# Optimization experiments

Hardware: AMD Instinct MI355X
Metric: run time of the kernel (lower is better)

The kernel has to match this reference:

```python
import jax, jax.numpy as jnp
import numpy as np

NUM_HEADS = 8
MASK_NEG = -1e30


def setup_inputs() -> dict:
    key = jax.random.key(0)
    k1, k2, k3 = jax.random.split(key, 3)
    B, S, D = 8, 2048, 128
    queries = jax.random.normal(k1, (B, S, D), dtype=jnp.float32)
    mask = jnp.ones((B, S), dtype=jnp.float32)
    # kernel_size=1 Conv1D with no bias == dense matmul over last dim
    W_q = jax.random.normal(k2, (D, D), dtype=jnp.float32) * (D ** -0.5)
    W_mem = jax.random.normal(k3, (D, 2 * D), dtype=jnp.float32) * (D ** -0.5)
    return {"queries": queries, "mask": mask, "W_q": W_q, "W_mem": W_mem}


def _split_heads(x, h):
    # [B, S, D] -> [B, h, S, D/h]
    B, S, D = x.shape
    return x.reshape(B, S, h, D // h).transpose(0, 2, 1, 3)


def reference(queries, mask, W_q, W_mem):
    B, S, D = queries.shape
    h = NUM_HEADS
    scale = (D // h) ** -0.5
    memory = jnp.einsum('bsd,de->bse', queries, W_mem)   # [B,S,2D]
    query = jnp.einsum('bsd,de->bse', queries, W_q)      # [B,S,D]
    K, V = jnp.split(memory, 2, axis=2)
    Q = _split_heads(query, h) * scale                   # [B,h,S,dh]
    K = _split_heads(K, h)
    V = _split_heads(V, h)
    logits = jnp.einsum('bhqd,bhkd->bhqk', Q, K)         # [B,h,S,S]
    m = mask.reshape(B, 1, 1, S)
    logits = logits + (1.0 - m) * MASK_NEG
    weights = jax.nn.softmax(logits, axis=-1)
    # dropout is identity at inference (training=None)
    x = jnp.einsum('bhqk,bhkd->bhqd', weights, V)        # [B,h,S,dh]
    return x.transpose(0, 2, 1, 3).reshape(B, S, D)
```

## Files before the change

kernel.cpp:

```cpp
#include <hip/hip_runtime.h>
#include <hip/hip_bf16.h>
#include <stdint.h>

#define B_    8
#define S_    2048
#define D_    128
#define H_    8
#define DH_   16
#define BH_   64
#define E_    384
#define NT_   (S_ / 32)

typedef __attribute__((ext_vector_type(4)))  short short4v;
typedef __attribute__((ext_vector_type(8)))  short short8;
typedef __attribute__((ext_vector_type(4)))  float f32x4;
typedef __attribute__((ext_vector_type(16))) float f32x16;

__device__ inline unsigned short f2b(float f) {
    union { __bf16 h; unsigned short u; } t;
    t.h = (__bf16)f;
    return t.u;
}
__device__ inline float b2f(unsigned short u) {
    union { unsigned u; float f; } x; x.u = ((unsigned)u) << 16; return x.f;
}
__device__ inline int dperm(int d) {
    return (d & 3) | ((d & 8) >> 1) | ((d & 4) << 1);
}

__device__ inline void gload_lds16(const void* g, void* l) {
    __builtin_amdgcn_global_load_lds(
        (const __attribute__((address_space(1))) unsigned int*)g,
        (__attribute__((address_space(3))) unsigned int*)l, 16, 0, 0);
}

#define EXPB 16250.7346f

__global__ void wtrans_kernel(const float* __restrict__ Wq,
                              const float* __restrict__ Wmem,
                              unsigned short* __restrict__ wt) {
    int e = blockIdx.x, k = threadIdx.x;
    float v = (e < 128) ? Wq[k * 128 + e] : Wmem[k * 256 + (e - 128)];
    wt[e * 128 + k] = f2b(v);
}

__global__ __launch_bounds__(512) void proj_kernel(
        const float* __restrict__ X, const float* __restrict__ mask,
        const unsigned short* __restrict__ wt,
        unsigned short* __restrict__ Qb, unsigned short* __restrict__ KVf) {
    __shared__ unsigned short Xs[64][136];
    __shared__ unsigned short Vs[64][136];
    __shared__ float Ms[64];
    const int tid = threadIdx.x;
    const int b = blockIdx.x & 7, st = blockIdx.x >> 3;
    const int s0 = st * 64;
    const float* Xp = X + ((size_t)b * S_ + s0) * D_;

    for (int i = tid; i < 64 * D_ / 4; i += 512) {
        f32x4 v = __builtin_nontemporal_load((const f32x4*)Xp + i);
        int row = i >> 5, c4 = (i & 31) * 4;
        Xs[row][c4 + 0] = f2b(v[0]); Xs[row][c4 + 1] = f2b(v[1]);
        Xs[row][c4 + 2] = f2b(v[2]); Xs[row][c4 + 3] = f2b(v[3]);
    }
    if (tid < 64) Ms[tid] = mask[(size_t)b * S_ + s0 + tid];
    __syncthreads();

    const int wid = tid >> 6, lane = tid & 63;
    const int lr = lane & 15, lg = lane >> 4;
    const float qscale = 0.25f * 1.44269504088896f;

    for (int ci = 0; ci < 3; ++ci) {
        const int ct = wid + ci * 8;
        const int e0 = ct * 16;
        short4v bfr[8];
        #pragma unroll
        for (int kk = 0; kk < 8; ++kk)
            bfr[kk] = *(const short4v*)&wt[(e0 + lr) * 128 + kk * 16 + lg * 4];
        for (int rt = 0; rt < 4; ++rt) {
            f32x4 acc; acc[0] = acc[1] = acc[2] = acc[3] = 0.f;
            #pragma unroll
            for (int kk = 0; kk < 8; ++kk) {
                short4v a = *(const short4v*)&Xs[rt * 16 + lr][kk * 16 + lg * 4];
                acc = __builtin_amdgcn_mfma_f32_16x16x16bf16_1k(a, bfr[kk], acc, 0, 0, 0);
            }
            const int e = e0 + lr;
            #pragma unroll
            for (int r = 0; r < 4; ++r) {
                const int sl = rt * 16 + lg * 4 + r;
                const float v = acc[r];
                if (e < 128) {
                    int hh = e >> 4, d = dperm(e & 15);
                    Qb[(((size_t)b * H_ + hh) * S_ + s0 + sl) * DH_ + d] = f2b(v * qscale);
                } else if (e < 256) {
                    int ek = e - 128, hh = ek >> 4, d = dperm(ek & 15);
                    int T = st * 2 + (sl >> 5), qq = sl & 31;
                    int l = qq + 32 * (d >> 3), j = d & 7;
                    KVf[((size_t)(b * H_ + hh) * NT_ + T) * 1536 + l * 8 + j] = f2b(v);
                } else {
                    Vs[sl][e - 256] = f2b(v);
                }
            }
        }
    }
    __syncthreads();

    for (int j = tid; j < H_ * 2 * 2 * 64; j += 512) {
        const int l = j & 63, f = (j >> 6) & 1, t = (j >> 7) & 1, hh = j >> 8;
        const int q = l & 31, h = l >> 5;
        const int vrow = (q < 16) ? q : 16;
        const int T = st * 2 + t;
        unsigned short* dst =
            KVf + ((size_t)(b * H_ + hh) * NT_ + T) * 1536 + (1 + f) * 512 + l * 8;
        union { unsigned short us[8]; short8 v; } o;
        #pragma unroll
        for (int e = 0; e < 8; ++e) {
            const int p = f * 16 + 8 * h + e;
            const int sl = (p & 16) | dperm(p & 15);
            const int srow = t * 32 + sl;
            const float mk = Ms[srow];
            o.us[e] = f2b((vrow == 16) ? mk : b2f(Vs[srow][hh * 16 + vrow]) * mk);
        }
        *(short8*)dst = o.v;
    }
}

__global__ __launch_bounds__(512, 6) void attn_kernel(
        const unsigned short* __restrict__ Qb, const unsigned short* __restrict__ KVf,
        float* __restrict__ out) {
    const int tid = threadIdx.x;
    const int wid = tid >> 6, lane = tid & 63;
    const int q = lane & 31, h = lane >> 5;
    const int p = blockIdx.x;
    const int bh = (p & 7) * 8 + ((p >> 3) & 7);
    const int qt = p >> 6;
    const int q0 = qt * 128 + (wid >> 1) * 32;
    const int ttBase = (wid & 1) * (NT_ / 2);
    const int ttEnd  = ttBase + NT_ / 2;

    __shared__ unsigned short lds[8][2][3][64][8];

    const unsigned short* kv = KVf + (size_t)bh * NT_ * 1536 + (size_t)lane * 8;

    const short8 qf = *(const short8*)&Qb[((size_t)bh * S_ + q0 + q) * DH_ + 8 * h];

    f32x16 acc, z;
    #pragma unroll
    for (int i = 0; i < 16; ++i) { acc[i] = 0.f; z[i] = 0.f; }

#define STAGE(TT_, SL_)                                                        \
    {                                                                          \
        const unsigned short* g_ = kv + (size_t)(TT_) * 1536;                  \
        gload_lds16(g_,        &lds[wid][SL_][0][0][0]);                       \
        gload_lds16(g_ + 512,  &lds[wid][SL_][1][0][0]);                       \
        gload_lds16(g_ + 1024, &lds[wid][SL_][2][0][0]);                       \
    }

    STAGE(ttBase, 0); STAGE(ttBase + 1, 1);

    #pragma unroll 2
    for (int j = 0; j < 32; ++j) {
        const int slot = j & 1;
        asm volatile("s_waitcnt vmcnt(3)" ::: "memory");
        __builtin_amdgcn_sched_barrier(0);
        const short8 kf  = *(const short8*)&lds[wid][slot][0][lane][0];
        const short8 va0 = *(const short8*)&lds[wid][slot][1][lane][0];
        const short8 va1 = *(const short8*)&lds[wid][slot][2][lane][0];
        asm volatile("s_waitcnt lgkmcnt(0)" ::: "memory");
        __builtin_amdgcn_sched_barrier(0);
        const int nt2 = ttBase + j + 2;
        STAGE(nt2 < ttEnd ? nt2 : nt2 - 32, slot);

        __builtin_amdgcn_s_setprio(1);
        f32x16 s0 = __builtin_amdgcn_mfma_f32_32x32x16_bf16(kf, qf, z, 0, 0, 0);
        __builtin_amdgcn_s_setprio(0);

        union { unsigned u[4]; short8 v; } b0, b1;
        #pragma unroll
        for (int i = 0; i < 4; ++i) {
            const int l0 = (int)__builtin_fmaf(s0[2 * i],     128.f, EXPB);
            const int h0 = (int)__builtin_fmaf(s0[2 * i + 1], 128.f, EXPB);
            b0.u[i] = (unsigned)l0 | ((unsigned)h0 << 16);
            const int l1 = (int)__builtin_fmaf(s0[8 + 2 * i],     128.f, EXPB);
            const int h1 = (int)__builtin_fmaf(s0[8 + 2 * i + 1], 128.f, EXPB);
            b1.u[i] = (unsigned)l1 | ((unsigned)h1 << 16);
        }
        __builtin_amdgcn_s_setprio(1);
        acc = __builtin_amdgcn_mfma_f32_32x32x16_bf16(va0, b0.v, acc, 0, 0, 0);
        acc = __builtin_amdgcn_mfma_f32_32x32x16_bf16(va1, b1.v, acc, 0, 0, 0);
        __builtin_amdgcn_s_setprio(0);
    }
#undef STAGE

    asm volatile("s_waitcnt vmcnt(0)" ::: "memory");
    __syncthreads();

    float (*cmb)[16][64] = (float (*)[16][64]) & lds[0][0][0][0][0];
    if (wid & 1) {
        #pragma unroll
        for (int i = 0; i < 16; ++i)
            cmb[wid >> 1][i][lane] = acc[i];
    }
    __syncthreads();
    if (!(wid & 1)) {
        const int b = bh >> 3, head = bh & 7;
        float* obase = out + ((size_t)b * S_ + q0 + q) * D_ + head * DH_ + 4 * h;
        float o[16];
        #pragma unroll
        for (int i = 0; i < 16; ++i) o[i] = acc[i] + cmb[wid >> 1][i][lane];
        const float r = 1.0f / o[8];
        *(float4*)obase       = make_float4(o[0] * r, o[1] * r, o[2] * r, o[3] * r);
        *(float4*)(obase + 8) = make_float4(o[4] * r, o[5] * r, o[6] * r, o[7] * r);
    }
}

extern "C" void kernel_launch(void* const* d_in, const int* in_sizes, int n_in,
                              void* d_out, int out_size, void* d_ws, size_t ws_size,
                              hipStream_t stream) {
    const float* X    = (const float*)d_in[0];
    const float* mask = (const float*)d_in[1];
    const float* Wq   = (const float*)d_in[2];
    const float* Wmem = (const float*)d_in[3];
    float* out = (float*)d_out;

    unsigned short* Qb  = (unsigned short*)d_ws;
    unsigned short* KVf = Qb + (size_t)BH_ * S_ * DH_;
    unsigned short* wt  = KVf + (size_t)BH_ * NT_ * 1536;

    wtrans_kernel<<<E_, 128, 0, stream>>>(Wq, Wmem, wt);
    proj_kernel<<<B_ * S_ / 64, 512, 0, stream>>>(X, mask, wt, Qb, KVf);
    attn_kernel<<<BH_ * (S_ / 128), 512, 0, stream>>>(Qb, KVf, out);
}
```

Measured before the change: 63.84 us.

## Share KV tiles across all waves in block via cooperative LDS staging

```diff
diff --git a/kernel.cpp b/kernel.cpp
--- a/kernel.cpp
+++ b/kernel.cpp
@@ -124,7 +124,7 @@
     }
 }
 
-__global__ __launch_bounds__(512, 6) void attn_kernel(
+__global__ __launch_bounds__(512, 4) void attn_kernel(
         const unsigned short* __restrict__ Qb, const unsigned short* __restrict__ KVf,
         float* __restrict__ out) {
     const int tid = threadIdx.x;
@@ -132,85 +132,83 @@
     const int q = lane & 31, h = lane >> 5;
     const int p = blockIdx.x;
     const int bh = (p & 7) * 8 + ((p >> 3) & 7);
-    const int qt = p >> 6;
-    const int q0 = qt * 128 + (wid >> 1) * 32;
-    const int ttBase = (wid & 1) * (NT_ / 2);
-    const int ttEnd  = ttBase + NT_ / 2;
-
-    __shared__ unsigned short lds[8][2][3][64][8];
+    const int qs = p >> 6;
+    const int q0 = qs * 256 + wid * 32;
+
+    __shared__ unsigned short buf[2][8][3][64][8];
 
     const unsigned short* kv = KVf + (size_t)bh * NT_ * 1536 + (size_t)lane * 8;
 
     const short8 qf = *(const short8*)&Qb[((size_t)bh * S_ + q0 + q) * DH_ + 8 * h];
 
-    f32x16 acc, z;
+    f32x16 accA, accB, z;
     #pragma unroll
-    for (int i = 0; i < 16; ++i) { acc[i] = 0.f; z[i] = 0.f; }
-
-#define STAGE(TT_, SL_)                                                        \
+    for (int i = 0; i < 16; ++i) { accA[i] = 0.f; accB[i] = 0.f; z[i] = 0.f; }
+
+#define STAGE(C_)                                                              \
     {                                                                          \
-        const unsigned short* g_ = kv + (size_t)(TT_) * 1536;                  \
-        gload_lds16(g_,        &lds[wid][SL_][0][0][0]);                       \
-        gload_lds16(g_ + 512,  &lds[wid][SL_][1][0][0]);                       \
-        gload_lds16(g_ + 1024, &lds[wid][SL_][2][0][0]);                       \
-    }
-
-    STAGE(ttBase, 0); STAGE(ttBase + 1, 1);
-
-    #pragma unroll 2
-    for (int j = 0; j < 32; ++j) {
-        const int slot = j & 1;
-        asm volatile("s_waitcnt vmcnt(3)" ::: "memory");
-        __builtin_amdgcn_sched_barrier(0);
-        const short8 kf  = *(const short8*)&lds[wid][slot][0][lane][0];
-        const short8 va0 = *(const short8*)&lds[wid][slot][1][lane][0];
-        const short8 va1 = *(const short8*)&lds[wid][slot][2][lane][0];
-        asm volatile("s_waitcnt lgkmcnt(0)" ::: "memory");
-        __builtin_amdgcn_sched_barrier(0);
-        const int nt2 = ttBase + j + 2;
-        STAGE(nt2 < ttEnd ? nt2 : nt2 - 32, slot);
-
-        __builtin_amdgcn_s_setprio(1);
-        f32x16 s0 = __builtin_amdgcn_mfma_f32_32x32x16_bf16(kf, qf, z, 0, 0, 0);
-        __builtin_amdgcn_s_setprio(0);
-
-        union { unsigned u[4]; short8 v; } b0, b1;
-        #pragma unroll
-        for (int i = 0; i < 4; ++i) {
-            const int l0 = (int)__builtin_fmaf(s0[2 * i],     128.f, EXPB);
-            const int h0 = (int)__builtin_fmaf(s0[2 * i + 1], 128.f, EXPB);
-            b0.u[i] = (unsigned)l0 | ((unsigned)h0 << 16);
-            const int l1 = (int)__builtin_fmaf(s0[8 + 2 * i],     128.f, EXPB);
-            const int h1 = (int)__builtin_fmaf(s0[8 + 2 * i + 1], 128.f, EXPB);
-            b1.u[i] = (unsigned)l1 | ((unsigned)h1 << 16);
-        }
-        __builtin_amdgcn_s_setprio(1);
-        acc = __builtin_amdgcn_mfma_f32_32x32x16_bf16(va0, b0.v, acc, 0, 0, 0);
-        acc = __builtin_amdgcn_mfma_f32_32x32x16_bf16(va1, b1.v, acc, 0, 0, 0);
-        __builtin_amdgcn_s_setprio(0);
+        const unsigned short* g_ = kv + (size_t)((C_) * 8 + wid) * 1536;       \
+        unsigned short* d_ = &buf[(C_) & 1][wid][0][0][0];                     \
+        gload_lds16(g_,        d_);                                            \
+        gload_lds16(g_ + 512,  d_ + 512);                                      \
+        gload_lds16(g_ + 1024, d_ + 1024);                                     \
+    }
+
+#define TILE_BODY(ACC_, BI_, T_)                                               \
+    {                                                                          \
+        const short8 kf  = *(const short8*)&buf[BI_][T_][0][lane][0];          \
+        const short8 va0 = *(const short8*)&buf[BI_][T_][1][lane][0];          \
+        const short8 va1 = *(const short8*)&buf[BI_][T_][2][lane][0];          \
+        __builtin_amdgcn_s_setprio(1);                                         \
+        f32x16 s0 = __builtin_amdgcn_mfma_f32_32x32x16_bf16(kf, qf, z, 0, 0, 0); \
+        __builtin_amdgcn_s_setprio(0);                                         \
+        union { unsigned u[4]; short8 v; } b0, b1;                             \
+        _Pragma("unroll")                                                      \
+        for (int i = 0; i < 4; ++i) {                                          \
+            const int l0 = (int)__builtin_fmaf(s0[2 * i],     128.f, EXPB);    \
+            const int h0 = (int)__builtin_fmaf(s0[2 * i + 1], 128.f, EXPB);    \
+            b0.u[i] = (unsigned)l0 | ((unsigned)h0 << 16);                     \
+            const int l1 = (int)__builtin_fmaf(s0[8 + 2 * i],     128.f, EXPB);\
+            const int h1 = (int)__builtin_fmaf(s0[8 + 2 * i + 1], 128.f, EXPB);\
+            b1.u[i] = (unsigned)l1 | ((unsigned)h1 << 16);                     \
+        }                                                                      \
+        __builtin_amdgcn_s_setprio(1);                                         \
+        ACC_ = __builtin_amdgcn_mfma_f32_32x32x16_bf16(va0, b0.v, ACC_, 0, 0, 0); \
+        ACC_ = __builtin_amdgcn_mfma_f32_32x32x16_bf16(va1, b1.v, ACC_, 0, 0, 0); \
+        __builtin_amdgcn_s_setprio(0);                                         \
+    }
+
+    STAGE(0);
+
+    for (int c = 0; c < 4; ++c) {
+        asm volatile("s_waitcnt vmcnt(0)" ::: "memory");
+        __builtin_amdgcn_s_barrier();
+        asm volatile("" ::: "memory");
+        STAGE(c + 1);
+        const int bi = c & 1;
+        #pragma unroll
+        for (int t = 0; t < 8; ++t) TILE_BODY(accA, bi, t);
+    }
+    for (int c = 4; c < 8; ++c) {
+        asm volatile("s_waitcnt vmcnt(0)" ::: "memory");
+        __builtin_amdgcn_s_barrier();
+        asm volatile("" ::: "memory");
+        if (c < 7) STAGE(c + 1);
+        const int bi = c & 1;
+        #pragma unroll
+        for (int t = 0; t < 8; ++t) TILE_BODY(accB, bi, t);
     }
 #undef STAGE
-
-    asm volatile("s_waitcnt vmcnt(0)" ::: "memory");
-    __syncthreads();
-
-    float (*cmb)[16][64] = (float (*)[16][64]) & lds[0][0][0][0][0];
-    if (wid & 1) {
-        #pragma unroll
-        for (int i = 0; i < 16; ++i)
-            cmb[wid >> 1][i][lane] = acc[i];
-    }
-    __syncthreads();
-    if (!(wid & 1)) {
-        const int b = bh >> 3, head = bh & 7;
-        float* obase = out + ((size_t)b * S_ + q0 + q) * D_ + head * DH_ + 4 * h;
-        float o[16];
-        #pragma unroll
-        for (int i = 0; i < 16; ++i) o[i] = acc[i] + cmb[wid >> 1][i][lane];
-        const float r = 1.0f / o[8];
-        *(float4*)obase       = make_float4(o[0] * r, o[1] * r, o[2] * r, o[3] * r);
-        *(float4*)(obase + 8) = make_float4(o[4] * r, o[5] * r, o[6] * r, o[7] * r);
-    }
+#undef TILE_BODY
+
+    const int b = bh >> 3, head = bh & 7;
+    float* obase = out + ((size_t)b * S_ + q0 + q) * D_ + head * DH_ + 4 * h;
+    float o[16];
+    #pragma unroll
+    for (int i = 0; i < 16; ++i) o[i] = accA[i] + accB[i];
+    const float r = 1.0f / o[8];
+    *(float4*)obase       = make_float4(o[0] * r, o[1] * r, o[2] * r, o[3] * r);
+    *(float4*)(obase + 8) = make_float4(o[4] * r, o[5] * r, o[6] * r, o[7] * r);
 }
 
 extern "C" void kernel_launch(void* const* d_in, const int* in_sizes, int n_in,
@@ -228,5 +226,5 @@
 
     wtrans_kernel<<<E_, 128, 0, stream>>>(Wq, Wmem, wt);
     proj_kernel<<<B_ * S_ / 64, 512, 0, stream>>>(X, mask, wt, Qb, KVf);
-    attn_kernel<<<BH_ * (S_ / 128), 512, 0, stream>>>(Qb, KVf, out);
-}
+    attn_kernel<<<BH_ * 8, 512, 0, stream>>>(Qb, KVf, out);
+}
```

Result: faster. 56.79 us (-11.0%).
